# Performance work log

Measured on AMD Instinct MI355X. Metric: run time of the kernel, lower is better.

Reference implementation:

```python
import jax, jax.numpy as jnp
import numpy as np

B, S, V, NC, CV, CE, WE, KS = 64, 256, 50000, 20, 256, 32, 512, 4


def setup_inputs() -> dict:
    key = jax.random.key(0)
    k1, k2, k3, k4 = jax.random.split(key, 4)
    data = jax.random.randint(k1, (B, S), 0, V, dtype=jnp.int32)
    spelling = jax.random.randint(k2, (V, NC), 0, CV, dtype=jnp.int32)
    char_emb_w = jax.random.normal(k3, (CV, CE), dtype=jnp.float32)
    cnn_w = jax.random.uniform(k4, (WE, CE + 1, KS), dtype=jnp.float32,
                               minval=-0.05, maxval=0.05)
    return {"char_emb_w": char_emb_w, "cnn_w": cnn_w,
            "data": data, "spelling": spelling}


def reference(char_emb_w, cnn_w, data, spelling):
    # spelling gather: [B,S] -> [B,S,NC] char ids -> [B,S,NC,CE] char embeddings
    sp = spelling[data]
    ce = char_emb_w[sp]
    bsz, seq_len, nc, ces = ce.shape
    x = ce.reshape(bsz * seq_len, nc, ces)
    # mode='l2' -> lang bit is 1.0 (would be 0.0 for 'l1')
    lang_bit = jnp.ones((bsz * seq_len, nc, 1), dtype=x.dtype)
    x = jnp.concatenate([x, lang_bit], axis=2).transpose(0, 2, 1)  # [N, CE+1, NC]
    # Conv1d, valid padding, no bias: [N, WE, NC-KS+1]
    y = jax.lax.conv_general_dilated(x, cnn_w, window_strides=(1,),
                                     padding='VALID',
                                     dimension_numbers=('NCH', 'OIH', 'NCH'))
    # MaxPool1d over full remaining length
    word_emb = jnp.max(y, axis=2)  # [N, WE]
    return word_emb.reshape(bsz, seq_len, -1)
```

## Files before the change

kernel.cpp:

```cpp
#include <hip/hip_runtime.h>
#include <hip/hip_bf16.h>
#include <cstdint>

#define NWORDS 16384
#define NCH    20
#define CEDIM  32
#define WEDIM  512
#define WPB    32
#define NBLK   (NWORDS/WPB)

typedef __attribute__((ext_vector_type(8)))  short bf16x8;
typedef __attribute__((ext_vector_type(16))) float f32x16;

__device__ __forceinline__ unsigned short f2bf(float f){
    union { float f; unsigned int u; } v; v.f = f;
    unsigned int u = v.u + 0x7fffu + ((v.u >> 16) & 1u);
    return (unsigned short)(u >> 16);
}

__global__ __launch_bounds__(256) void prep_kernel(const float* __restrict__ cnn,
                                                   const float* __restrict__ cemb,
                                                   unsigned short* __restrict__ wbf3,
                                                   unsigned short* __restrict__ cembbf,
                                                   float* __restrict__ bias){
    int idx = blockIdx.x * 256 + threadIdx.x;
    if (idx < 65536){
        int j   = idx & 7;
        int col = (idx >> 3) & 31;
        int lh  = (idx >> 8) & 1;
        int s   = (idx >> 9) & 7;
        int cc  = idx >> 12;
        int o   = cc*32 + col;
        int kk  = s*16 + lh*8 + j;
        int i   = kk & 31, k = kk >> 5;
        wbf3[idx] = f2bf(cnn[o*132 + i*4 + k]);
    } else if (idx < 65536 + 256*CEDIM){
        int r = idx - 65536;
        cembbf[r] = f2bf(cemb[r]);
    } else if (idx < 65536 + 256*CEDIM + WEDIM){
        int o = idx - (65536 + 256*CEDIM);
        const float* p = cnn + o*132 + 128;
        bias[o] = p[0] + p[1] + p[2] + p[3];
    }
}

__global__ __attribute__((amdgpu_waves_per_eu(2))) __launch_bounds__(512)
void conv_kernel(
    const int* __restrict__ data,
    const int* __restrict__ spelling,
    const unsigned short* __restrict__ cembbf,
    const unsigned short* __restrict__ wbf3,
    const float* __restrict__ bias,
    float* __restrict__ out)
{
    __shared__ __align__(16) char sA[20*4*32*16];

    const int tid  = threadIdx.x;
    const int wv   = tid >> 6;
    const int lane = tid & 63;
    const int ln31 = lane & 31;
    const int lh   = lane >> 5;
    const int wbase = blockIdx.x * WPB;

    {
        auto stage = [&](int c, int w){
            int wd = data[wbase + w];
            int id = spelling[wd*NCH + c];
            const uint4* src = reinterpret_cast<const uint4*>(cembbf + id*CEDIM);
            #pragma unroll
            for (int q = 0; q < 4; ++q){
                uint4 v = src[q];
                *reinterpret_cast<uint4*>(sA + ((c*4 + q) << 9) + (w << 4)) = v;
            }
        };
        stage(tid >> 5, tid & 31);
        if (tid < 128) stage(16 + (tid >> 5), tid & 31);
    }
    __syncthreads();

    const char* wb = (const char*)wbf3;

    auto ldA = [&](int c, int p) -> bf16x8 {
        return *reinterpret_cast<const bf16x8*>(
            sA + ((c*4 + p*2 + lh) << 9) + (ln31 << 4));
    };

    f32x16 zz;
    #pragma unroll
    for (int r = 0; r < 16; ++r) zz[r] = 0.f;

    #pragma unroll 1
    for (int half = 0; half < 2; ++half){
        const int cc16 = wv + half*8;
        const int colb = cc16*32;

        const char* wbb = wb + cc16*8192 + lane*16;
        bf16x8 bs[8];
        #pragma unroll
        for (int s = 0; s < 8; ++s)
            bs[s] = *reinterpret_cast<const bf16x8*>(wbb + s*1024);

        bf16x8 aw[4][2];
        #pragma unroll
        for (int c = 0; c < 4; ++c){
            aw[c][0] = ldA(c, 0);
            aw[c][1] = ldA(c, 1);
        }

        f32x16 vmax;
        #pragma unroll
        for (int t = 0; t < 17; ++t){
            f32x16 acc;
            acc = __builtin_amdgcn_mfma_f32_32x32x16_bf16(aw[ t   &3][0], bs[0], zz,  0,0,0);
            acc = __builtin_amdgcn_mfma_f32_32x32x16_bf16(aw[ t   &3][1], bs[1], acc, 0,0,0);
            acc = __builtin_amdgcn_mfma_f32_32x32x16_bf16(aw[(t+1)&3][0], bs[2], acc, 0,0,0);
            acc = __builtin_amdgcn_mfma_f32_32x32x16_bf16(aw[(t+1)&3][1], bs[3], acc, 0,0,0);
            acc = __builtin_amdgcn_mfma_f32_32x32x16_bf16(aw[(t+2)&3][0], bs[4], acc, 0,0,0);
            acc = __builtin_amdgcn_mfma_f32_32x32x16_bf16(aw[(t+2)&3][1], bs[5], acc, 0,0,0);
            acc = __builtin_amdgcn_mfma_f32_32x32x16_bf16(aw[(t+3)&3][0], bs[6], acc, 0,0,0);
            acc = __builtin_amdgcn_mfma_f32_32x32x16_bf16(aw[(t+3)&3][1], bs[7], acc, 0,0,0);

            if (t == 0){
                vmax = acc;
            } else {
                #pragma unroll
                for (int r = 0; r < 16; ++r) vmax[r] = fmaxf(vmax[r], acc[r]);
            }
            if (t < 16){
                aw[t&3][0] = ldA(t+4, 0);
                aw[t&3][1] = ldA(t+4, 1);
            }
        }

        float bv = bias[colb + ln31];
        #pragma unroll
        for (int r = 0; r < 16; ++r){
            int row = (r & 3) + 8*(r >> 2) + 4*lh;
            __builtin_nontemporal_store(vmax[r] + bv,
                out + (wbase + row)*WEDIM + colb + ln31);
        }
    }
}

extern "C" void kernel_launch(void* const* d_in, const int* in_sizes, int n_in,
                              void* d_out, int out_size, void* d_ws, size_t ws_size,
                              hipStream_t stream) {
    const float* cemb     = (const float*)d_in[0];
    const float* cnn      = (const float*)d_in[1];
    const int*   data     = (const int*)d_in[2];
    const int*   spelling = (const int*)d_in[3];
    float* outp = (float*)d_out;

    unsigned short* wbf3   = (unsigned short*)d_ws;
    float*          bias   = (float*)((char*)d_ws + 131072);
    unsigned short* cembbf = (unsigned short*)((char*)d_ws + 133120);

    int prep_items = 65536 + 256*CEDIM + WEDIM;
    prep_kernel<<<dim3((prep_items + 255)/256), dim3(256), 0, stream>>>(cnn, cemb, wbf3, cembbf, bias);
    conv_kernel<<<dim3(NBLK), dim3(512), 0, stream>>>(data, spelling, cembbf, wbf3, bias, outp);
}
```

Baseline: 102.8 us.

## Pre-gather transposed spelling ids and stage char embeddings via direct global-to-LDS loads

```diff
diff --git a/kernel.cpp b/kernel.cpp
--- a/kernel.cpp
+++ b/kernel.cpp
@@ -20,9 +20,12 @@
 
 __global__ __launch_bounds__(256) void prep_kernel(const float* __restrict__ cnn,
                                                    const float* __restrict__ cemb,
+                                                   const int* __restrict__ data,
+                                                   const int* __restrict__ spelling,
                                                    unsigned short* __restrict__ wbf3,
                                                    unsigned short* __restrict__ cembbf,
-                                                   float* __restrict__ bias){
+                                                   float* __restrict__ bias,
+                                                   int* __restrict__ spidsT){
     int idx = blockIdx.x * 256 + threadIdx.x;
     if (idx < 65536){
         int j   = idx & 7;
@@ -41,13 +44,23 @@
         int o = idx - (65536 + 256*CEDIM);
         const float* p = cnn + o*132 + 128;
         bias[o] = p[0] + p[1] + p[2] + p[3];
+    } else if (idx < 65536 + 256*CEDIM + WEDIM + NWORDS){
+        int w  = idx - (65536 + 256*CEDIM + WEDIM);
+        int wd = data[w];
+        const int4* sp = reinterpret_cast<const int4*>(spelling + wd*NCH);
+        int4 v0 = sp[0], v1 = sp[1], v2 = sp[2], v3 = sp[3], v4 = sp[4];
+        int vals[20] = { v0.x,v0.y,v0.z,v0.w, v1.x,v1.y,v1.z,v1.w,
+                         v2.x,v2.y,v2.z,v2.w, v3.x,v3.y,v3.z,v3.w,
+                         v4.x,v4.y,v4.z,v4.w };
+        #pragma unroll
+        for (int c = 0; c < NCH; ++c)
+            spidsT[c*NWORDS + w] = vals[c];
     }
 }
 
-__global__ __attribute__((amdgpu_waves_per_eu(2))) __launch_bounds__(512)
+__global__ __attribute__((amdgpu_waves_per_eu(2))) __launch_bounds__(256)
 void conv_kernel(
-    const int* __restrict__ data,
-    const int* __restrict__ spelling,
+    const int* __restrict__ spids,
     const unsigned short* __restrict__ cembbf,
     const unsigned short* __restrict__ wbf3,
     const float* __restrict__ bias,
@@ -63,18 +76,22 @@
     const int wbase = blockIdx.x * WPB;
 
     {
-        auto stage = [&](int c, int w){
-            int wd = data[wbase + w];
-            int id = spelling[wd*NCH + c];
-            const uint4* src = reinterpret_cast<const uint4*>(cembbf + id*CEDIM);
-            #pragma unroll
-            for (int q = 0; q < 4; ++q){
-                uint4 v = src[q];
-                *reinterpret_cast<uint4*>(sA + ((c*4 + q) << 9) + (w << 4)) = v;
-            }
-        };
-        stage(tid >> 5, tid & 31);
-        if (tid < 128) stage(16 + (tid >> 5), tid & 31);
+        int ids[10];
+        #pragma unroll
+        for (int n = 0; n < 10; ++n){
+            int cq = 2*(wv + 4*n) + lh;
+            ids[n] = spids[(cq >> 2)*NWORDS + wbase + ln31];
+        }
+        #pragma unroll
+        for (int n = 0; n < 10; ++n){
+            int pp = wv + 4*n;
+            int q  = (2*pp + lh) & 3;
+            const char* src = (const char*)cembbf + (ids[n] << 6) + (q << 4);
+            __builtin_amdgcn_global_load_lds(
+                (const __attribute__((address_space(1))) unsigned int*)src,
+                (__attribute__((address_space(3))) unsigned int*)(sA + (pp << 10)),
+                16, 0, 0);
+        }
     }
     __syncthreads();
 
@@ -90,8 +107,8 @@
     for (int r = 0; r < 16; ++r) zz[r] = 0.f;
 
     #pragma unroll 1
-    for (int half = 0; half < 2; ++half){
-        const int cc16 = wv + half*8;
+    for (int half = 0; half < 4; ++half){
+        const int cc16 = wv + half*4;
         const int colb = cc16*32;
 
         const char* wbb = wb + cc16*8192 + lane*16;
@@ -154,8 +171,10 @@
     unsigned short* wbf3   = (unsigned short*)d_ws;
     float*          bias   = (float*)((char*)d_ws + 131072);
     unsigned short* cembbf = (unsigned short*)((char*)d_ws + 133120);
+    int*            spids  = (int*)((char*)d_ws + 149504);
 
-    int prep_items = 65536 + 256*CEDIM + WEDIM;
-    prep_kernel<<<dim3((prep_items + 255)/256), dim3(256), 0, stream>>>(cnn, cemb, wbf3, cembbf, bias);
-    conv_kernel<<<dim3(NBLK), dim3(512), 0, stream>>>(data, spelling, cembbf, wbf3, bias, outp);
+    int prep_items = 65536 + 256*CEDIM + WEDIM + NWORDS;
+    prep_kernel<<<dim3((prep_items + 255)/256), dim3(256), 0, stream>>>(
+        cnn, cemb, data, spelling, wbf3, cembbf, bias, spids);
+    conv_kernel<<<dim3(NBLK), dim3(256), 0, stream>>>(spids, cembbf, wbf3, bias, outp);
 }
```

Result: no change. 101.9 us (-0.8%).
